# Kernel tuning notes

Hardware: AMD Instinct MI355X
Metric: run time of the kernel (lower is better)

Reference implementation:

```python
import jax, jax.numpy as jnp
from jax import lax
import numpy as np

DN = ('NCHW', 'OIHW', 'NCHW')

def conv(x, w, b, stride, pad):
    y = lax.conv_general_dilated(x, w, (stride, stride), [(pad, pad), (pad, pad)], dimension_numbers=DN)
    return y + b[None, :, None, None]

def conv_t(x, w, b, stride, pad):
    # PyTorch ConvTranspose2d weight layout is (in, out, kh, kw); flip spatially, swap to OIHW,
    # and realize transpose-conv as lhs-dilated conv with padding k-1-p.
    k = w.shape[2]
    wt = jnp.flip(w, (2, 3)).transpose(1, 0, 2, 3)
    q = k - 1 - pad
    y = lax.conv_general_dilated(x, wt, (1, 1), [(q, q), (q, q)], lhs_dilation=(stride, stride), dimension_numbers=DN)
    return y + b[None, :, None, None]

def setup_inputs() -> dict:
    key = jax.random.key(0)
    ks = jax.random.split(key, 16)
    K, C = 512, 64
    def he(k, shape, fan_in):
        return jax.random.normal(k, shape, jnp.float32) * np.float32(np.sqrt(2.0 / fan_in))
    return {
        'x': jax.random.normal(ks[0], (64, 1, 256, 256), jnp.float32),
        'e1_w': he(ks[1], (32, 1, 4, 4), 1 * 16), 'e1_b': jnp.zeros((32,), jnp.float32),
        'e2_w': he(ks[2], (64, 32, 4, 4), 32 * 16), 'e2_b': jnp.zeros((64,), jnp.float32),
        'e3_w': he(ks[3], (64, 64, 3, 3), 64 * 9), 'e3_b': jnp.zeros((64,), jnp.float32),
        'emb': jax.random.uniform(ks[4], (K, C), jnp.float32, -1.0 / K, 1.0 / K),
        'd1_w': he(ks[5], (64, 32, 3, 3), 64 * 9), 'd1_b': jnp.zeros((32,), jnp.float32),
        'd2_w': he(ks[6], (32, 64, 4, 4), 32 * 16), 'd2_b': jnp.zeros((64,), jnp.float32),
        'd3_w': he(ks[7], (64, 1, 4, 4), 64 * 16), 'd3_b': jnp.zeros((1,), jnp.float32),
    }

def reference(x, e1_w, e1_b, e2_w, e2_b, e3_w, e3_b, emb, d1_w, d1_b, d2_w, d2_b, d3_w, d3_b):
    # encoder
    h = jax.nn.relu(conv(x, e1_w, e1_b, 2, 1))
    h = jax.nn.relu(conv(h, e2_w, e2_b, 2, 1))
    ze = jax.nn.relu(conv(h, e3_w, e3_b, 1, 1))  # (N, C, H, W)
    N, C, H, W = ze.shape
    # VQ: nearest codebook entry per spatial location via ||z||^2 - 2 z.e + ||e||^2
    zf = ze.transpose(0, 2, 3, 1).reshape(-1, C)  # (N*H*W, C)
    dist = (zf * zf).sum(-1, keepdims=True) - 2.0 * (zf @ emb.T) + (emb * emb).sum(-1)[None, :]
    idx = jnp.argmin(dist, axis=1)  # (N*H*W,)
    zq = emb[idx].reshape(N, H, W, C).transpose(0, 3, 1, 2)  # (N, C, H, W)
    # straight-through estimator
    dec_in = ze + lax.stop_gradient(zq - ze)
    # decoder
    h = jax.nn.relu(conv_t(dec_in, d1_w, d1_b, 1, 1))
    h = jax.nn.relu(conv_t(h, d2_w, d2_b, 2, 1))
    x_hat = conv_t(h, d3_w, d3_b, 2, 1)
    return (x_hat, ze, zq)
```

## Files before the change

### kernel.cpp

```cpp
#include <hip/hip_runtime.h>

typedef short short8 __attribute__((ext_vector_type(8)));
typedef float f32x4 __attribute__((ext_vector_type(4)));

__device__ __forceinline__ unsigned short f2bf(float f) {
    unsigned int u = __float_as_uint(f);
    u = (u + 0x7fffu + ((u >> 16) & 1u)) >> 16;
    return (unsigned short)u;
}
__device__ __forceinline__ float bf2f(unsigned short s) {
    return __uint_as_float(((unsigned int)s) << 16);
}


__global__ __launch_bounds__(256) void k_init(
    unsigned int* __restrict__ ws_dw,
    const float* __restrict__ e2w, const float* __restrict__ e3w,
    const float* __restrict__ d1w, const float* __restrict__ d2w,
    const float* __restrict__ d3w, const float* __restrict__ emb,
    unsigned short* __restrict__ ape2, unsigned short* __restrict__ ape3,
    unsigned short* __restrict__ apd1, unsigned short* __restrict__ apd2,
    unsigned short* __restrict__ apd3, unsigned short* __restrict__ embbf,
    float* __restrict__ hninit)
{
    int bid = blockIdx.x;
    if (bid < 7280) {
        int t = bid * 256 + threadIdx.x;
        if (t < 270336) {
            int img = t / 4224, q = t % 4224;
            int rowsel = q / 2112, rem = q % 2112;
            ws_dw[img * 274560 + rowsel * 129 * 2112 + rem] = 0u;
        } else if (t < 532480) {
            int g = t - 270336;
            int img = g / 4096, q = g % 4096;
            int row = 1 + (q >> 5), c2 = q & 31;
            int sel = c2 >> 4, ch = c2 & 15;
            int par = sel ? 0 : 1, idx = sel ? 64 : 0;
            ws_dw[img * 274560 + row * 2112 + par * 1056 + idx * 16 + ch] = 0u;
        } else if (t < 1863680) {
            unsigned int base, Cd, r;
            if (t < 1064960)      { base = 17571840u; Cd = 32; r = t - 532480;  }
            else if (t < 1597440) { base = 34881536u; Cd = 32; r = t - 1064960; }
            else                  { base = 43802624u; Cd = 16; r = t - 1597440; }
            unsigned int per_img = 260u * Cd;
            unsigned int img = r / per_img, q = r % per_img;
            unsigned int p = q / Cd, c = q % Cd;
            unsigned int row, col;
            if (p < 66u)        { row = 0;  col = p; }
            else if (p < 132u)  { row = 65; col = p - 66u; }
            else { unsigned int s = p - 132u; row = 1 + (s >> 1); col = (s & 1) ? 65u : 0u; }
            ws_dw[base + ((img * 66u + row) * 66u + col) * Cd + c] = 0u;
        }
        return;
    }
    int f = (bid - 7280) * 256 + threadIdx.x;
    if (f < 4096) {
        int ks = f >> 8, mt = (f >> 6) & 3, lane = f & 63;
        int quad = lane >> 4, l16 = lane & 15;
        int oc = mt * 16 + l16, kh = ks >> 2, kw = ks & 3;
        short8 sv;
#pragma unroll
        for (int j = 0; j < 8; j++) {
            int ic = quad * 8 + j;
            sv[j] = (short)f2bf(e2w[((oc * 32 + ic) * 4 + kh) * 4 + kw]);
        }
        ((short8*)ape2)[f] = sv;
    } else if (f < 8704) {
        int g = f - 4096;
        int ks = g >> 8, mt = (g >> 6) & 3, lane = g & 63;
        int quad = lane >> 4, l16 = lane & 15;
        int oc = mt * 16 + l16, tap = ks >> 1, kh = tap / 3, kw = tap % 3;
        int icb = (ks & 1) * 32 + quad * 8;
        short8 sv;
#pragma unroll
        for (int j = 0; j < 8; j++)
            sv[j] = (short)f2bf(e3w[((oc * 64 + icb + j) * 3 + kh) * 3 + kw]);
        ((short8*)ape3)[g] = sv;
    } else if (f < 11008) {
        int g = f - 8704;
        int ks = g >> 7, mt = (g >> 6) & 1, lane = g & 63;
        int quad = lane >> 4, l16 = lane & 15;
        int oc = mt * 16 + l16, tap = ks >> 1, kh = tap / 3, kw = tap % 3;
        int icb = (ks & 1) * 32 + quad * 8;
        short8 sv;
#pragma unroll
        for (int j = 0; j < 8; j++)
            sv[j] = (short)f2bf(d1w[(((icb + j) * 32 + oc) * 3 + (2 - kh)) * 3 + (2 - kw)]);
        ((short8*)apd1)[g] = sv;
    } else if (f < 15104) {
        int g = f - 11008;
        int par = g >> 10, ks = (g >> 8) & 3, mt = (g >> 6) & 3, lane = g & 63;
        int quad = lane >> 4, l16 = lane & 15;
        int ph = par >> 1, pw = par & 1, a = ks >> 1, bb = ks & 1;
        int kh = 3 - ph - 2 * a, kw = 3 - pw - 2 * bb;
        int oc = mt * 16 + l16;
        short8 sv;
#pragma unroll
        for (int j = 0; j < 8; j++) {
            int ic = quad * 8 + j;
            sv[j] = (short)f2bf(d2w[((ic * 64 + oc) * 4 + kh) * 4 + kw]);
        }
        ((short8*)apd2)[g] = sv;
    } else if (f < 15232) {
        int g = f - 15104;
        int ks = g >> 6, lane = g & 63;
        int quad = lane >> 4, tap = lane & 15;
        short8 sv;
#pragma unroll
        for (int j = 0; j < 8; j++) {
            int ic = ks * 32 + quad * 8 + j;
            sv[j] = (short)f2bf(d3w[ic * 16 + tap]);
        }
        ((short8*)apd3)[g] = sv;
    } else if (f < 19328) {
        int g = f - 15232;
        int code = g >> 3, chb = (g & 7) * 8;
        short8 sv;
#pragma unroll
        for (int j = 0; j < 8; j++) sv[j] = (short)f2bf(emb[code * 64 + chb + j]);
        ((short8*)embbf)[g] = sv;
    } else if (f < 19840) {
        int code = f - 19328;
        float s = 0.f;
        for (int c = 0; c < 64; c++) { float v = emb[code * 64 + c]; s += v * v; }
        hninit[code] = 2.0f - 0.5f * s;
    }
}

__global__ __launch_bounds__(256) void k_e1(const float* __restrict__ x,
                                            const float* __restrict__ w,
                                            const float* __restrict__ b,
                                            unsigned short* __restrict__ h1p2) {
    int idx = blockIdx.x * 256 + threadIdx.x;
    int ow = idx & 127, oh = (idx >> 7) & 127, n = idx >> 14;
    const float* xn = x + (size_t)n * 65536;
    float patch[16];
#pragma unroll
    for (int kh = 0; kh < 4; kh++) {
        int ih = 2 * oh + kh - 1;
#pragma unroll
        for (int kw = 0; kw < 4; kw++) {
            int iw = 2 * ow + kw - 1;
            bool ok = ((unsigned)ih < 256u) & ((unsigned)iw < 256u);
            patch[kh * 4 + kw] = ok ? xn[ih * 256 + iw] : 0.f;
        }
    }
    unsigned int outw[16];
#pragma unroll
    for (int oc = 0; oc < 32; oc++) {
        float acc = b[oc];
#pragma unroll
        for (int t = 0; t < 16; t++) acc += patch[t] * w[oc * 16 + t];
        unsigned short bf = f2bf(fmaxf(acc, 0.f));
        if (oc & 1) outw[oc >> 1] |= ((unsigned int)bf) << 16;
        else        outw[oc >> 1] = bf;
    }
    int par = ow & 1;
    int cidx = (ow + par) >> 1;
    size_t base = ((size_t)(n * 130 + oh + 1) * 2 + par) * 2112 + cidx * 32;
    uint4* dst = (uint4*)(h1p2 + base);
#pragma unroll
    for (int i = 0; i < 4; i++) dst[i] = *(uint4*)&outw[i * 4];
}

template<int CIN, int COUT, int KSTEPS, int NCH, int WPIN, int MODE>
__global__ __launch_bounds__(256) void k_conv(const unsigned short* __restrict__ inp,
                                              const unsigned short* __restrict__ aprep,
                                              const float* __restrict__ bias,
                                              unsigned short* __restrict__ out0,
                                              float* __restrict__ out1,
                                              unsigned short* __restrict__ out2) {
    constexpr int MT = COUT / 16;
    constexpr int KCH = KSTEPS / NCH;
    __shared__ short8 sA[KCH * MT * 64];
    int tid = threadIdx.x;
    int wave = tid >> 6, lane = tid & 63, quad = lane >> 4, l16 = lane & 15;
    int bid = blockIdx.x;
    int n = bid >> 4, rg = bid & 15;
    int oh = rg * 4 + wave;

    int base0;
    if (MODE == 0) base0 = (n * 130 + 2 * oh) * 4224 + quad * 8;
    else           base0 = n * (WPIN * WPIN * CIN) + ((oh + 1) * WPIN + 1) * CIN + quad * 8;

    f32x4 acc[4][MT];
#pragma unroll
    for (int t = 0; t < 4; t++)
#pragma unroll
        for (int mt = 0; mt < MT; mt++)
            acc[t][mt] = *(const f32x4*)(bias + mt * 16 + quad * 4);

#pragma unroll
    for (int ch = 0; ch < NCH; ch++) {
        for (int i = tid; i < KCH * MT * 64; i += 256)
            sA[i] = ((const short8*)aprep)[ch * (KCH * MT * 64) + i];
        __syncthreads();
#pragma unroll
        for (int k = 0; k < KCH; k++) {
            int ks = ch * KCH + k;
            int off, pxs;
            if (MODE == 0) {
                int kh = ks >> 2, kw = ks & 3;
                int par = (kw & 1) ^ 1;
                off = kh * 4224 + par * 2112 + (kw >> 1) * 32;
                pxs = 32;
            } else {
                int tap = ks >> 1, kh = tap / 3, kw = tap % 3;
                off = ((kh - 1) * WPIN + (kw - 1)) * CIN + (ks & 1) * 32;
                pxs = CIN;
            }
            short8 bfr[4];
#pragma unroll
            for (int t = 0; t < 4; t++)
                bfr[t] = *(const short8*)(inp + base0 + (t * 16 + l16) * pxs + off);
#pragma unroll
            for (int mt = 0; mt < MT; mt++) {
                short8 a = sA[(k * MT + mt) * 64 + lane];
#pragma unroll
                for (int t = 0; t < 4; t++)
                    acc[t][mt] = __builtin_amdgcn_mfma_f32_16x16x32_bf16(a, bfr[t], acc[t][mt], 0, 0, 0);
            }
        }
        if (ch + 1 < NCH) __syncthreads();
    }

#pragma unroll
    for (int t = 0; t < 4; t++) {
        int ow = t * 16 + l16;
#pragma unroll
        for (int mt = 0; mt < MT; mt++) {
            float v0 = fmaxf(acc[t][mt][0], 0.f), v1 = fmaxf(acc[t][mt][1], 0.f);
            float v2 = fmaxf(acc[t][mt][2], 0.f), v3 = fmaxf(acc[t][mt][3], 0.f);
            unsigned int lo = (unsigned int)f2bf(v0) | ((unsigned int)f2bf(v1) << 16);
            unsigned int hi = (unsigned int)f2bf(v2) | ((unsigned int)f2bf(v3) << 16);
            uint2 uu; uu.x = lo; uu.y = hi;
            int oc = mt * 16 + quad * 4;
            if (MODE == 0) {
                size_t addr = (size_t)n * 278784 + ((oh + 1) * 66 + ow + 1) * 64 + oc;
                *(uint2*)(out0 + addr) = uu;
            } else if (MODE == 1) {
                int px = oh * 64 + ow;
                __builtin_nontemporal_store(v0, &out1[((size_t)n * 64 + oc + 0) * 4096 + px]);
                __builtin_nontemporal_store(v1, &out1[((size_t)n * 64 + oc + 1) * 4096 + px]);
                __builtin_nontemporal_store(v2, &out1[((size_t)n * 64 + oc + 2) * 4096 + px]);
                __builtin_nontemporal_store(v3, &out1[((size_t)n * 64 + oc + 3) * 4096 + px]);
                size_t addr = ((size_t)n * 4096 + px) * 64 + oc;
                *(uint2*)(out2 + addr) = uu;
            } else {
                size_t addr = (size_t)n * 139392 + ((oh + 1) * 66 + ow + 1) * 32 + oc;
                *(uint2*)(out0 + addr) = uu;
            }
        }
    }
}

__global__ __launch_bounds__(512) void k_vq(const unsigned short* __restrict__ zeN,
                                            const unsigned short* __restrict__ embbf,
                                            const float* __restrict__ hninit,
                                            float* __restrict__ zq_out,
                                            unsigned short* __restrict__ zqp) {
    __shared__ short8 semb[4096];
    int tid = threadIdx.x;
    int wave = tid >> 6, lane = tid & 63, quad = lane >> 4, l16 = lane & 15;
    for (int i = tid; i < 4096; i += 512) semb[i] = ((const short8*)embbf)[i];
    __syncthreads();

    int pxb = blockIdx.x * 512 + wave * 64;
    short8 b0[4], b1[4];
#pragma unroll
    for (int t = 0; t < 4; t++) {
        int px = pxb + t * 16 + l16;
        b0[t] = *(const short8*)(zeN + (size_t)px * 64 + quad * 8);
        b1[t] = *(const short8*)(zeN + (size_t)px * 64 + 32 + quad * 8);
    }
    unsigned int bk[4] = {0u, 0u, 0u, 0u};
#pragma unroll 4
    for (int j0 = 0; j0 < 512; j0 += 16) {
        short8 a0 = semb[(j0 + l16) * 8 + quad];
        short8 a1 = semb[(j0 + l16) * 8 + 4 + quad];
        f32x4 ci = *(const f32x4*)(hninit + j0 + quad * 4);
        int iv = 511 - j0 - quad * 4;
#pragma unroll
        for (int t = 0; t < 4; t++) {
            f32x4 s = __builtin_amdgcn_mfma_f32_16x16x32_bf16(a0, b0[t], ci, 0, 0, 0);
            s = __builtin_amdgcn_mfma_f32_16x16x32_bf16(a1, b1[t], s, 0, 0, 0);
#pragma unroll
            for (int r = 0; r < 4; r++) {
                unsigned int key = (__float_as_uint(s[r]) & 0xFFFFFE00u) | (unsigned int)(iv - r);
                bk[t] = bk[t] > key ? bk[t] : key;
            }
        }
    }
#pragma unroll
    for (int t = 0; t < 4; t++) {
        unsigned int o1 = (unsigned int)__shfl_xor((int)bk[t], 16);
        bk[t] = bk[t] > o1 ? bk[t] : o1;
        unsigned int o2 = (unsigned int)__shfl_xor((int)bk[t], 32);
        bk[t] = bk[t] > o2 ? bk[t] : o2;
    }
#pragma unroll
    for (int t = 0; t < 4; t++) {
        int code = 511 - (int)(bk[t] & 511u);
        int px = pxb + t * 16 + l16;
        int n = px >> 12, hw = px & 4095, h = hw >> 6, w = hw & 63;
        uint4 u0 = *(const uint4*)&semb[code * 8 + quad * 2];
        uint4 u1 = *(const uint4*)&semb[code * 8 + quad * 2 + 1];
        size_t qaddr = (size_t)n * 278784 + ((h + 1) * 66 + (w + 1)) * 64 + quad * 16;
        *(uint4*)(zqp + qaddr) = u0;
        *(uint4*)(zqp + qaddr + 8) = u1;
        size_t zb = ((size_t)n * 64 + quad * 16) * 4096 + hw;
        unsigned int uw[8] = {u0.x, u0.y, u0.z, u0.w, u1.x, u1.y, u1.z, u1.w};
#pragma unroll
        for (int i = 0; i < 8; i++) {
            __builtin_nontemporal_store(__uint_as_float(uw[i] << 16), &zq_out[zb + (2 * i + 0) * 4096]);
            __builtin_nontemporal_store(__uint_as_float(uw[i] & 0xFFFF0000u), &zq_out[zb + (2 * i + 1) * 4096]);
        }
    }
}

__global__ __launch_bounds__(256) void k_d2f(const unsigned short* __restrict__ d1op,
                                             const unsigned short* __restrict__ apd2,
                                             const float* __restrict__ bias,
                                             const unsigned short* __restrict__ apd3,
                                             unsigned short* __restrict__ sc16) {
    __shared__ short8 sA[1024];
    __shared__ short  sT[4 * 64 * 72];
    int tid = threadIdx.x;
    int wave = tid >> 6, lane = tid & 63, quad = lane >> 4, l16 = lane & 15;
    int bid = blockIdx.x;
    int n = bid >> 6, par = (bid >> 4) & 3, rg = bid & 15;
    int oh = rg * 4 + wave;
    int ph = par >> 1, pw = par & 1;

    for (int i = tid; i < 1024; i += 256) sA[i] = ((const short8*)apd2)[par * 1024 + i];
    __syncthreads();

    int base0 = n * 139392 + ((oh + ph) * 66 + pw) * 32 + quad * 8;
    f32x4 acc[4][4];
#pragma unroll
    for (int t = 0; t < 4; t++)
#pragma unroll
        for (int mt = 0; mt < 4; mt++)
            acc[t][mt] = *(const f32x4*)(bias + mt * 16 + quad * 4);

#pragma unroll
    for (int k = 0; k < 4; k++) {
        int a_ = k >> 1, bb = k & 1;
        int off = (a_ * 66 + bb) * 32;
        short8 bfr[4];
#pragma unroll
        for (int t = 0; t < 4; t++)
            bfr[t] = *(const short8*)(d1op + base0 + (t * 16 + l16) * 32 + off);
#pragma unroll
        for (int mt = 0; mt < 4; mt++) {
            short8 a = sA[(k * 4 + mt) * 64 + lane];
#pragma unroll
            for (int t = 0; t < 4; t++)
                acc[t][mt] = __builtin_amdgcn_mfma_f32_16x16x32_bf16(a, bfr[t], acc[t][mt], 0, 0, 0);
        }
    }
#pragma unroll
    for (int t = 0; t < 4; t++) {
#pragma unroll
        for (int mt = 0; mt < 4; mt++) {
            float v0 = fmaxf(acc[t][mt][0], 0.f), v1 = fmaxf(acc[t][mt][1], 0.f);
            float v2 = fmaxf(acc[t][mt][2], 0.f), v3 = fmaxf(acc[t][mt][3], 0.f);
            uint2 uu;
            uu.x = (unsigned int)f2bf(v0) | ((unsigned int)f2bf(v1) << 16);
            uu.y = (unsigned int)f2bf(v2) | ((unsigned int)f2bf(v3) << 16);
            int addr = wave * 4608 + (t * 16 + l16) * 72 + mt * 16 + quad * 4;
            *(uint2*)&sT[addr] = uu;
        }
    }
    __syncthreads();
    short8 pa0 = ((const short8*)apd3)[lane];
    short8 pa1 = ((const short8*)apd3)[64 + lane];
    int oh_out = 2 * oh + ph;
#pragma unroll
    for (int t = 0; t < 4; t++) {
        const short* pbase = &sT[wave * 4608 + (t * 16 + l16) * 72];
        short8 pb0 = *(const short8*)(pbase + quad * 8);
        short8 pb1 = *(const short8*)(pbase + 32 + quad * 8);
        f32x4 sc = {0.f, 0.f, 0.f, 0.f};
        sc = __builtin_amdgcn_mfma_f32_16x16x32_bf16(pa0, pb0, sc, 0, 0, 0);
        sc = __builtin_amdgcn_mfma_f32_16x16x32_bf16(pa1, pb1, sc, 0, 0, 0);
        int ow_out = 2 * (t * 16 + l16) + pw;
        int pbaseo = n * 16384 + oh_out * 128 + ow_out;
#pragma unroll
        for (int r = 0; r < 4; r++) {
            int tap = quad * 4 + r;
            sc16[(size_t)tap * 1048576 + pbaseo] = f2bf(sc[r]);
        }
    }
}

__global__ __launch_bounds__(256) void k_d3e(const unsigned short* __restrict__ sc16,
                                             const float* __restrict__ d3b,
                                             float* __restrict__ xhat) {
    int idx = blockIdx.x * 256 + threadIdx.x;
    int ow = idx & 255, oh = (idx >> 8) & 255, n = idx >> 16;
    float acc = d3b[0];
    int kh0 = (oh + 1) & 1, kw0 = (ow + 1) & 1;
#pragma unroll
    for (int dh = 0; dh < 2; dh++) {
        int kh = kh0 + 2 * dh;
        int ih = (oh + 1 - kh) >> 1;
        bool vh = ((unsigned)ih < 128u);
#pragma unroll
        for (int dw = 0; dw < 2; dw++) {
            int kw = kw0 + 2 * dw;
            int iw = (ow + 1 - kw) >> 1;
            if (vh && ((unsigned)iw < 128u))
                acc += bf2f(sc16[(size_t)(kh * 4 + kw) * 1048576 + n * 16384 + ih * 128 + iw]);
        }
    }
    __builtin_nontemporal_store(acc, &xhat[(size_t)n * 65536 + oh * 256 + ow]);
}

extern "C" void kernel_launch(void* const* d_in, const int* in_sizes, int n_in,
                              void* d_out, int out_size, void* d_ws, size_t ws_size,
                              hipStream_t stream) {
    const float* x    = (const float*)d_in[0];
    const float* e1w  = (const float*)d_in[1];
    const float* e1b  = (const float*)d_in[2];
    const float* e2w  = (const float*)d_in[3];
    const float* e2b  = (const float*)d_in[4];
    const float* e3w  = (const float*)d_in[5];
    const float* e3b  = (const float*)d_in[6];
    const float* emb  = (const float*)d_in[7];
    const float* d1w  = (const float*)d_in[8];
    const float* d1b  = (const float*)d_in[9];
    const float* d2w  = (const float*)d_in[10];
    const float* d2b  = (const float*)d_in[11];
    const float* d3w  = (const float*)d_in[12];
    const float* d3b  = (const float*)d_in[13];

    float* xhat = (float*)d_out;
    float* ze   = xhat + 4194304;
    float* zq   = ze + 16777216;

    char* ws = (char*)d_ws;
    unsigned short* h1p2   = (unsigned short*)(ws + 0);
    unsigned short* h2p    = (unsigned short*)(ws + 70287360);
    unsigned short* zeN    = (unsigned short*)(ws + 105971712);
    unsigned short* zqp    = (unsigned short*)(ws + 139526144);
    unsigned short* d1op   = (unsigned short*)(ws + 175210496);
    unsigned short* sc16   = (unsigned short*)(ws + 193052672);
    unsigned short* ape2   = (unsigned short*)(ws + 226607104);
    unsigned short* ape3   = (unsigned short*)(ws + 226672640);
    unsigned short* apd1   = (unsigned short*)(ws + 226746368);
    unsigned short* apd2   = (unsigned short*)(ws + 226783232);
    unsigned short* apd3   = (unsigned short*)(ws + 226848768);
    unsigned short* embbf  = (unsigned short*)(ws + 226850816);
    float*          hninit = (float*)(ws + 226916352);

    k_init<<<7358, 256, 0, stream>>>((unsigned int*)d_ws, e2w, e3w, d1w, d2w, d3w, emb,
                                     ape2, ape3, apd1, apd2, apd3, embbf, hninit);
    k_e1<<<4096, 256, 0, stream>>>(x, e1w, e1b, h1p2);
    k_conv<32, 64, 16, 2, 0, 0><<<1024, 256, 0, stream>>>(h1p2, ape2, e2b, h2p, nullptr, nullptr);
    k_conv<64, 64, 18, 2, 66, 1><<<1024, 256, 0, stream>>>(h2p, ape3, e3b, nullptr, ze, zeN);
    k_vq<<<512, 512, 0, stream>>>(zeN, embbf, hninit, zq, zqp);
    k_conv<64, 32, 18, 2, 66, 2><<<1024, 256, 0, stream>>>(zqp, apd1, d1b, d1op, nullptr, nullptr);
    k_d2f<<<4096, 256, 0, stream>>>(d1op, apd2, d2b, apd3, sc16);
    k_d3e<<<16384, 256, 0, stream>>>(sc16, d3b, xhat);
}
```

Baseline: 432.1 us.

## Fuse e3 conv with VQ, merge e1 into init, shuffle-based d2f epilogue

Merges the e1 convolution into the init kernel so both run in one launch. Fuses the e3 convolution with the VQ codebook search, using cross-lane shuffles to reshape MFMA accumulators into B operands, which removes the zeN round trip through global memory and one launch. The codebook is now read from global/L2 instead of LDS. The d2f epilogue likewise drops its LDS transpose and barrier in favour of register shuffles, and launch bounds request 3 blocks per CU. The cost is higher register pressure and codebook reads that no longer come from LDS inside the VQ loop.

```diff
diff --git a/kernel.cpp b/kernel.cpp
--- a/kernel.cpp
+++ b/kernel.cpp
@@ -2,6 +2,8 @@
 
 typedef short short8 __attribute__((ext_vector_type(8)));
 typedef float f32x4 __attribute__((ext_vector_type(4)));
+
+union U8 { short8 s8; unsigned int u[4]; };
 
 __device__ __forceinline__ unsigned short f2bf(float f) {
     unsigned int u = __float_as_uint(f);
@@ -13,8 +15,9 @@
 }
 
 
-__global__ __launch_bounds__(256) void k_init(
-    unsigned int* __restrict__ ws_dw,
+__global__ __launch_bounds__(256) void k_e1i(
+    const float* __restrict__ x, const float* __restrict__ e1w, const float* __restrict__ e1b,
+    unsigned short* __restrict__ h1p2, unsigned int* __restrict__ ws_dw,
     const float* __restrict__ e2w, const float* __restrict__ e3w,
     const float* __restrict__ d1w, const float* __restrict__ d2w,
     const float* __restrict__ d3w, const float* __restrict__ emb,
@@ -24,8 +27,41 @@
     float* __restrict__ hninit)
 {
     int bid = blockIdx.x;
-    if (bid < 7280) {
-        int t = bid * 256 + threadIdx.x;
+    if (bid < 4096) {
+        int idx = bid * 256 + threadIdx.x;
+        int ow = idx & 127, oh = (idx >> 7) & 127, n = idx >> 14;
+        const float* xn = x + (size_t)n * 65536;
+        float patch[16];
+#pragma unroll
+        for (int kh = 0; kh < 4; kh++) {
+            int ih = 2 * oh + kh - 1;
+#pragma unroll
+            for (int kw = 0; kw < 4; kw++) {
+                int iw = 2 * ow + kw - 1;
+                bool ok = ((unsigned)ih < 256u) & ((unsigned)iw < 256u);
+                patch[kh * 4 + kw] = ok ? xn[ih * 256 + iw] : 0.f;
+            }
+        }
+        unsigned int outw[16];
+#pragma unroll
+        for (int oc = 0; oc < 32; oc++) {
+            float acc = e1b[oc];
+#pragma unroll
+            for (int t = 0; t < 16; t++) acc += patch[t] * e1w[oc * 16 + t];
+            unsigned short bf = f2bf(fmaxf(acc, 0.f));
+            if (oc & 1) outw[oc >> 1] |= ((unsigned int)bf) << 16;
+            else        outw[oc >> 1] = bf;
+        }
+        int par = ow & 1;
+        int cidx = (ow + par) >> 1;
+        size_t base = ((size_t)((idx >> 14) * 130 + oh + 1) * 2 + par) * 2112 + cidx * 32;
+        uint4* dst = (uint4*)(h1p2 + base);
+#pragma unroll
+        for (int i = 0; i < 4; i++) dst[i] = *(uint4*)&outw[i * 4];
+        return;
+    }
+    if (bid < 11376) {
+        int t = (bid - 4096) * 256 + threadIdx.x;
         if (t < 270336) {
             int img = t / 4224, q = t % 4224;
             int rowsel = q / 2112, rem = q % 2112;
@@ -35,8 +71,8 @@
             int img = g / 4096, q = g % 4096;
             int row = 1 + (q >> 5), c2 = q & 31;
             int sel = c2 >> 4, ch = c2 & 15;
-            int par = sel ? 0 : 1, idx = sel ? 64 : 0;
-            ws_dw[img * 274560 + row * 2112 + par * 1056 + idx * 16 + ch] = 0u;
+            int par = sel ? 0 : 1, idx2 = sel ? 64 : 0;
+            ws_dw[img * 274560 + row * 2112 + par * 1056 + idx2 * 16 + ch] = 0u;
         } else if (t < 1863680) {
             unsigned int base, Cd, r;
             if (t < 1064960)      { base = 17571840u; Cd = 32; r = t - 532480;  }
@@ -53,7 +89,7 @@
         }
         return;
     }
-    int f = (bid - 7280) * 256 + threadIdx.x;
+    int f = (bid - 11376) * 256 + threadIdx.x;
     if (f < 4096) {
         int ks = f >> 8, mt = (f >> 6) & 3, lane = f & 63;
         int quad = lane >> 4, l16 = lane & 15;
@@ -127,49 +163,11 @@
     }
 }
 
-__global__ __launch_bounds__(256) void k_e1(const float* __restrict__ x,
-                                            const float* __restrict__ w,
-                                            const float* __restrict__ b,
-                                            unsigned short* __restrict__ h1p2) {
-    int idx = blockIdx.x * 256 + threadIdx.x;
-    int ow = idx & 127, oh = (idx >> 7) & 127, n = idx >> 14;
-    const float* xn = x + (size_t)n * 65536;
-    float patch[16];
-#pragma unroll
-    for (int kh = 0; kh < 4; kh++) {
-        int ih = 2 * oh + kh - 1;
-#pragma unroll
-        for (int kw = 0; kw < 4; kw++) {
-            int iw = 2 * ow + kw - 1;
-            bool ok = ((unsigned)ih < 256u) & ((unsigned)iw < 256u);
-            patch[kh * 4 + kw] = ok ? xn[ih * 256 + iw] : 0.f;
-        }
-    }
-    unsigned int outw[16];
-#pragma unroll
-    for (int oc = 0; oc < 32; oc++) {
-        float acc = b[oc];
-#pragma unroll
-        for (int t = 0; t < 16; t++) acc += patch[t] * w[oc * 16 + t];
-        unsigned short bf = f2bf(fmaxf(acc, 0.f));
-        if (oc & 1) outw[oc >> 1] |= ((unsigned int)bf) << 16;
-        else        outw[oc >> 1] = bf;
-    }
-    int par = ow & 1;
-    int cidx = (ow + par) >> 1;
-    size_t base = ((size_t)(n * 130 + oh + 1) * 2 + par) * 2112 + cidx * 32;
-    uint4* dst = (uint4*)(h1p2 + base);
-#pragma unroll
-    for (int i = 0; i < 4; i++) dst[i] = *(uint4*)&outw[i * 4];
-}
-
 template<int CIN, int COUT, int KSTEPS, int NCH, int WPIN, int MODE>
-__global__ __launch_bounds__(256) void k_conv(const unsigned short* __restrict__ inp,
-                                              const unsigned short* __restrict__ aprep,
-                                              const float* __restrict__ bias,
-                                              unsigned short* __restrict__ out0,
-                                              float* __restrict__ out1,
-                                              unsigned short* __restrict__ out2) {
+__global__ __launch_bounds__(256, 3) void k_conv(const unsigned short* __restrict__ inp,
+                                                 const unsigned short* __restrict__ aprep,
+                                                 const float* __restrict__ bias,
+                                                 unsigned short* __restrict__ out0) {
     constexpr int MT = COUT / 16;
     constexpr int KCH = KSTEPS / NCH;
     __shared__ short8 sA[KCH * MT * 64];
@@ -238,14 +236,6 @@
             if (MODE == 0) {
                 size_t addr = (size_t)n * 278784 + ((oh + 1) * 66 + ow + 1) * 64 + oc;
                 *(uint2*)(out0 + addr) = uu;
-            } else if (MODE == 1) {
-                int px = oh * 64 + ow;
-                __builtin_nontemporal_store(v0, &out1[((size_t)n * 64 + oc + 0) * 4096 + px]);
-                __builtin_nontemporal_store(v1, &out1[((size_t)n * 64 + oc + 1) * 4096 + px]);
-                __builtin_nontemporal_store(v2, &out1[((size_t)n * 64 + oc + 2) * 4096 + px]);
-                __builtin_nontemporal_store(v3, &out1[((size_t)n * 64 + oc + 3) * 4096 + px]);
-                size_t addr = ((size_t)n * 4096 + px) * 64 + oc;
-                *(uint2*)(out2 + addr) = uu;
             } else {
                 size_t addr = (size_t)n * 139392 + ((oh + 1) * 66 + ow + 1) * 32 + oc;
                 *(uint2*)(out0 + addr) = uu;
@@ -254,30 +244,98 @@
     }
 }
 
-__global__ __launch_bounds__(512) void k_vq(const unsigned short* __restrict__ zeN,
-                                            const unsigned short* __restrict__ embbf,
-                                            const float* __restrict__ hninit,
-                                            float* __restrict__ zq_out,
-                                            unsigned short* __restrict__ zqp) {
-    __shared__ short8 semb[4096];
+__global__ __launch_bounds__(256, 3) void k_e3vq(const unsigned short* __restrict__ h2p,
+                                                 const unsigned short* __restrict__ ape3,
+                                                 const float* __restrict__ bias,
+                                                 const unsigned short* __restrict__ embbf,
+                                                 const float* __restrict__ hninit,
+                                                 float* __restrict__ ze_out,
+                                                 float* __restrict__ zq_out,
+                                                 unsigned short* __restrict__ zqp) {
+    __shared__ short8 sA[9 * 4 * 64];
     int tid = threadIdx.x;
     int wave = tid >> 6, lane = tid & 63, quad = lane >> 4, l16 = lane & 15;
-    for (int i = tid; i < 4096; i += 512) semb[i] = ((const short8*)embbf)[i];
-    __syncthreads();
-
-    int pxb = blockIdx.x * 512 + wave * 64;
+    int bid = blockIdx.x;
+    int n = bid >> 4, rg = bid & 15;
+    int oh = rg * 4 + wave;
+    int base0 = n * 278784 + ((oh + 1) * 66 + 1) * 64 + quad * 8;
+
+    f32x4 acc[4][4];
+#pragma unroll
+    for (int t = 0; t < 4; t++)
+#pragma unroll
+        for (int mt = 0; mt < 4; mt++)
+            acc[t][mt] = *(const f32x4*)(bias + mt * 16 + quad * 4);
+
+#pragma unroll
+    for (int ch = 0; ch < 2; ch++) {
+        for (int i = tid; i < 9 * 4 * 64; i += 256)
+            sA[i] = ((const short8*)ape3)[ch * (9 * 4 * 64) + i];
+        __syncthreads();
+#pragma unroll
+        for (int k = 0; k < 9; k++) {
+            int ks = ch * 9 + k;
+            int tap = ks >> 1, kh = tap / 3, kw = tap % 3;
+            int off = ((kh - 1) * 66 + (kw - 1)) * 64 + (ks & 1) * 32;
+            short8 bfr[4];
+#pragma unroll
+            for (int t = 0; t < 4; t++)
+                bfr[t] = *(const short8*)(h2p + base0 + (t * 16 + l16) * 64 + off);
+#pragma unroll
+            for (int mt = 0; mt < 4; mt++) {
+                short8 a = sA[(k * 4 + mt) * 64 + lane];
+#pragma unroll
+                for (int t = 0; t < 4; t++)
+                    acc[t][mt] = __builtin_amdgcn_mfma_f32_16x16x32_bf16(a, bfr[t], acc[t][mt], 0, 0, 0);
+            }
+        }
+        if (ch == 0) __syncthreads();
+    }
+
+#pragma unroll
+    for (int t = 0; t < 4; t++)
+#pragma unroll
+        for (int mt = 0; mt < 4; mt++)
+#pragma unroll
+            for (int r = 0; r < 4; r++)
+                acc[t][mt][r] = fmaxf(acc[t][mt][r], 0.f);
+
+#pragma unroll
+    for (int t = 0; t < 4; t++) {
+        int px = oh * 64 + t * 16 + l16;
+#pragma unroll
+        for (int mt = 0; mt < 4; mt++) {
+            int oc = mt * 16 + quad * 4;
+#pragma unroll
+            for (int r = 0; r < 4; r++)
+                __builtin_nontemporal_store(acc[t][mt][r], &ze_out[((size_t)n * 64 + oc + r) * 4096 + px]);
+        }
+    }
+
     short8 b0[4], b1[4];
+    int s0 = (((2 * quad) & 3) << 4) | l16;
+    int s1 = (((2 * quad + 1) & 3) << 4) | l16;
 #pragma unroll
     for (int t = 0; t < 4; t++) {
-        int px = pxb + t * 16 + l16;
-        b0[t] = *(const short8*)(zeN + (size_t)px * 64 + quad * 8);
-        b1[t] = *(const short8*)(zeN + (size_t)px * 64 + 32 + quad * 8);
-    }
+        f32x4 xv = (quad < 2) ? acc[t][0] : acc[t][1];
+        f32x4 yv = (quad < 2) ? acc[t][2] : acc[t][3];
+        unsigned int xa = (unsigned int)f2bf(xv[0]) | ((unsigned int)f2bf(xv[1]) << 16);
+        unsigned int xb = (unsigned int)f2bf(xv[2]) | ((unsigned int)f2bf(xv[3]) << 16);
+        unsigned int ya = (unsigned int)f2bf(yv[0]) | ((unsigned int)f2bf(yv[1]) << 16);
+        unsigned int yb = (unsigned int)f2bf(yv[2]) | ((unsigned int)f2bf(yv[3]) << 16);
+        U8 ub0, ub1;
+        ub0.u[0] = (unsigned int)__shfl((int)xa, s0); ub0.u[1] = (unsigned int)__shfl((int)xb, s0);
+        ub0.u[2] = (unsigned int)__shfl((int)xa, s1); ub0.u[3] = (unsigned int)__shfl((int)xb, s1);
+        ub1.u[0] = (unsigned int)__shfl((int)ya, s0); ub1.u[1] = (unsigned int)__shfl((int)yb, s0);
+        ub1.u[2] = (unsigned int)__shfl((int)ya, s1); ub1.u[3] = (unsigned int)__shfl((int)yb, s1);
+        b0[t] = ub0.s8; b1[t] = ub1.s8;
+    }
+
     unsigned int bk[4] = {0u, 0u, 0u, 0u};
 #pragma unroll 4
     for (int j0 = 0; j0 < 512; j0 += 16) {
-        short8 a0 = semb[(j0 + l16) * 8 + quad];
-        short8 a1 = semb[(j0 + l16) * 8 + 4 + quad];
+        short8 a0 = *(const short8*)(embbf + (j0 + l16) * 64 + quad * 8);
+        short8 a1 = *(const short8*)(embbf + (j0 + l16) * 64 + 32 + quad * 8);
         f32x4 ci = *(const f32x4*)(hninit + j0 + quad * 4);
         int iv = 511 - j0 - quad * 4;
 #pragma unroll
@@ -301,11 +359,11 @@
 #pragma unroll
     for (int t = 0; t < 4; t++) {
         int code = 511 - (int)(bk[t] & 511u);
-        int px = pxb + t * 16 + l16;
-        int n = px >> 12, hw = px & 4095, h = hw >> 6, w = hw & 63;
-        uint4 u0 = *(const uint4*)&semb[code * 8 + quad * 2];
-        uint4 u1 = *(const uint4*)&semb[code * 8 + quad * 2 + 1];
-        size_t qaddr = (size_t)n * 278784 + ((h + 1) * 66 + (w + 1)) * 64 + quad * 16;
+        int col = t * 16 + l16;
+        int hw = oh * 64 + col;
+        uint4 u0 = *(const uint4*)(embbf + code * 64 + quad * 16);
+        uint4 u1 = *(const uint4*)(embbf + code * 64 + quad * 16 + 8);
+        size_t qaddr = (size_t)n * 278784 + ((oh + 1) * 66 + (col + 1)) * 64 + quad * 16;
         *(uint4*)(zqp + qaddr) = u0;
         *(uint4*)(zqp + qaddr + 8) = u1;
         size_t zb = ((size_t)n * 64 + quad * 16) * 4096 + hw;
@@ -318,13 +376,12 @@
     }
 }
 
-__global__ __launch_bounds__(256) void k_d2f(const unsigned short* __restrict__ d1op,
-                                             const unsigned short* __restrict__ apd2,
-                                             const float* __restrict__ bias,
-                                             const unsigned short* __restrict__ apd3,
-                                             unsigned short* __restrict__ sc16) {
+__global__ __launch_bounds__(256, 3) void k_d2f(const unsigned short* __restrict__ d1op,
+                                                const unsigned short* __restrict__ apd2,
+                                                const float* __restrict__ bias,
+                                                const unsigned short* __restrict__ apd3,
+                                                unsigned short* __restrict__ sc16) {
     __shared__ short8 sA[1024];
-    __shared__ short  sT[4 * 64 * 72];
     int tid = threadIdx.x;
     int wave = tid >> 6, lane = tid & 63, quad = lane >> 4, l16 = lane & 15;
     int bid = blockIdx.x;
@@ -332,6 +389,9 @@
     int oh = rg * 4 + wave;
     int ph = par >> 1, pw = par & 1;
 
+    short8 pa0 = ((const short8*)apd3)[lane];
+    short8 pa1 = ((const short8*)apd3)[64 + lane];
+
     for (int i = tid; i < 1024; i += 256) sA[i] = ((const short8*)apd2)[par * 1024 + i];
     __syncthreads();
 
@@ -359,31 +419,31 @@
                 acc[t][mt] = __builtin_amdgcn_mfma_f32_16x16x32_bf16(a, bfr[t], acc[t][mt], 0, 0, 0);
         }
     }
+
+    int s0 = (((2 * quad) & 3) << 4) | l16;
+    int s1 = (((2 * quad + 1) & 3) << 4) | l16;
+    int oh_out = 2 * oh + ph;
 #pragma unroll
     for (int t = 0; t < 4; t++) {
 #pragma unroll
-        for (int mt = 0; mt < 4; mt++) {
-            float v0 = fmaxf(acc[t][mt][0], 0.f), v1 = fmaxf(acc[t][mt][1], 0.f);
-            float v2 = fmaxf(acc[t][mt][2], 0.f), v3 = fmaxf(acc[t][mt][3], 0.f);
-            uint2 uu;
-            uu.x = (unsigned int)f2bf(v0) | ((unsigned int)f2bf(v1) << 16);
-            uu.y = (unsigned int)f2bf(v2) | ((unsigned int)f2bf(v3) << 16);
-            int addr = wave * 4608 + (t * 16 + l16) * 72 + mt * 16 + quad * 4;
-            *(uint2*)&sT[addr] = uu;
-        }
-    }
-    __syncthreads();
-    short8 pa0 = ((const short8*)apd3)[lane];
-    short8 pa1 = ((const short8*)apd3)[64 + lane];
-    int oh_out = 2 * oh + ph;
-#pragma unroll
-    for (int t = 0; t < 4; t++) {
-        const short* pbase = &sT[wave * 4608 + (t * 16 + l16) * 72];
-        short8 pb0 = *(const short8*)(pbase + quad * 8);
-        short8 pb1 = *(const short8*)(pbase + 32 + quad * 8);
+        for (int mt = 0; mt < 4; mt++)
+#pragma unroll
+            for (int r = 0; r < 4; r++)
+                acc[t][mt][r] = fmaxf(acc[t][mt][r], 0.f);
+        f32x4 xv = (quad < 2) ? acc[t][0] : acc[t][1];
+        f32x4 yv = (quad < 2) ? acc[t][2] : acc[t][3];
+        unsigned int xa = (unsigned int)f2bf(xv[0]) | ((unsigned int)f2bf(xv[1]) << 16);
+        unsigned int xb = (unsigned int)f2bf(xv[2]) | ((unsigned int)f2bf(xv[3]) << 16);
+        unsigned int ya = (unsigned int)f2bf(yv[0]) | ((unsigned int)f2bf(yv[1]) << 16);
+        unsigned int yb = (unsigned int)f2bf(yv[2]) | ((unsigned int)f2bf(yv[3]) << 16);
+        U8 ub0, ub1;
+        ub0.u[0] = (unsigned int)__shfl((int)xa, s0); ub0.u[1] = (unsigned int)__shfl((int)xb, s0);
+        ub0.u[2] = (unsigned int)__shfl((int)xa, s1); ub0.u[3] = (unsigned int)__shfl((int)xb, s1);
+        ub1.u[0] = (unsigned int)__shfl((int)ya, s0); ub1.u[1] = (unsigned int)__shfl((int)yb, s0);
+        ub1.u[2] = (unsigned int)__shfl((int)ya, s1); ub1.u[3] = (unsigned int)__shfl((int)yb, s1);
         f32x4 sc = {0.f, 0.f, 0.f, 0.f};
-        sc = __builtin_amdgcn_mfma_f32_16x16x32_bf16(pa0, pb0, sc, 0, 0, 0);
-        sc = __builtin_amdgcn_mfma_f32_16x16x32_bf16(pa1, pb1, sc, 0, 0, 0);
+        sc = __builtin_amdgcn_mfma_f32_16x16x32_bf16(pa0, ub0.s8, sc, 0, 0, 0);
+        sc = __builtin_amdgcn_mfma_f32_16x16x32_bf16(pa1, ub1.s8, sc, 0, 0, 0);
         int ow_out = 2 * (t * 16 + l16) + pw;
         int pbaseo = n * 16384 + oh_out * 128 + ow_out;
 #pragma unroll
@@ -442,7 +502,6 @@
     char* ws = (char*)d_ws;
     unsigned short* h1p2   = (unsigned short*)(ws + 0);
     unsigned short* h2p    = (unsigned short*)(ws + 70287360);
-    unsigned short* zeN    = (unsigned short*)(ws + 105971712);
     unsigned short* zqp    = (unsigned short*)(ws + 139526144);
     unsigned short* d1op   = (unsigned short*)(ws + 175210496);
     unsigned short* sc16   = (unsigned short*)(ws + 193052672);
@@ -454,13 +513,12 @@
     unsigned short* embbf  = (unsigned short*)(ws + 226850816);
     float*          hninit = (float*)(ws + 226916352);
 
-    k_init<<<7358, 256, 0, stream>>>((unsigned int*)d_ws, e2w, e3w, d1w, d2w, d3w, emb,
+    k_e1i<<<11454, 256, 0, stream>>>(x, e1w, e1b, h1p2, (unsigned int*)d_ws,
+                                     e2w, e3w, d1w, d2w, d3w, emb,
                                      ape2, ape3, apd1, apd2, apd3, embbf, hninit);
-    k_e1<<<4096, 256, 0, stream>>>(x, e1w, e1b, h1p2);
-    k_conv<32, 64, 16, 2, 0, 0><<<1024, 256, 0, stream>>>(h1p2, ape2, e2b, h2p, nullptr, nullptr);
-    k_conv<64, 64, 18, 2, 66, 1><<<1024, 256, 0, stream>>>(h2p, ape3, e3b, nullptr, ze, zeN);
-    k_vq<<<512, 512, 0, stream>>>(zeN, embbf, hninit, zq, zqp);
-    k_conv<64, 32, 18, 2, 66, 2><<<1024, 256, 0, stream>>>(zqp, apd1, d1b, d1op, nullptr, nullptr);
+    k_conv<32, 64, 16, 2, 0, 0><<<1024, 256, 0, stream>>>(h1p2, ape2, e2b, h2p);
+    k_e3vq<<<1024, 256, 0, stream>>>(h2p, ape3, e3b, embbf, hninit, ze, zq, zqp);
+    k_conv<64, 32, 18, 2, 66, 2><<<1024, 256, 0, stream>>>(zqp, apd1, d1b, d1op);
     k_d2f<<<4096, 256, 0, stream>>>(d1op, apd2, d2b, apd3, sc16);
     k_d3e<<<16384, 256, 0, stream>>>(sc16, d3b, xhat);
 }
```

After: 429.5 us. About the same (-0.6%).
